# Performance work log

Hardware: AMD Instinct MI355X
Metric: run time of the kernel (lower is better)

## Reference

```python
import jax, jax.numpy as jnp
import numpy as np

OUT_F, IN_F = 4096, 11008
NUMEL = OUT_F * IN_F            # divisible by 256
NUM_SUPER = NUMEL // 256        # super-blocks of 8 sub-blocks x 32 values


def setup_inputs() -> dict:
    key = jax.random.key(0)
    k = jax.random.split(key, 7)
    x = jax.random.normal(k[0], (64, IN_F), dtype=jnp.float32)
    packed = jax.random.randint(k[1], (NUMEL // 2,), 0, 256, dtype=jnp.int32)
    d = jax.random.uniform(k[2], (NUM_SUPER,), dtype=jnp.float32) * 0.02
    dmin = jax.random.uniform(k[3], (NUM_SUPER,), dtype=jnp.float32) * 0.02
    scales = jax.random.randint(k[4], (NUM_SUPER * 8,), 0, 64, dtype=jnp.int32)
    mins = jax.random.randint(k[5], (NUM_SUPER * 8,), 0, 64, dtype=jnp.int32)
    bias = jax.random.normal(k[6], (OUT_F,), dtype=jnp.float32) * 0.02
    return {"x": x, "packed": packed, "d": d, "dmin": dmin,
            "scales": scales, "mins": mins, "bias": bias}


def _dequant_q4k(packed, d, dmin, scales, mins):
    # unpack two 4-bit quants per byte, interleaved low/high (stack dim=1 + flatten)
    low = packed & 15
    high = (packed >> 4) & 15
    q = jnp.stack([low, high], axis=1).reshape(NUM_SUPER, 8, 32).astype(jnp.float32)
    sc = (scales.astype(jnp.float32) / 63.0).reshape(NUM_SUPER, 8, 1)
    mn = (mins.astype(jnp.float32) / 63.0).reshape(NUM_SUPER, 8, 1)
    normalized = q / 15.0 * sc + mn
    w = normalized * d.reshape(NUM_SUPER, 1, 1) + dmin.reshape(NUM_SUPER, 1, 1)
    return w.reshape(OUT_F, IN_F)


def reference(x, packed, d, dmin, scales, mins, bias):
    w = _dequant_q4k(packed, d, dmin, scales, mins)   # [OUT_F, IN_F] fp32
    return x @ w.T + bias                              # F.linear
```

## Files before the change

kernel.cpp:

```cpp
#include <hip/hip_runtime.h>
#include <stdint.h>

#define OUT_F   4096
#define IN_F    11008
#define BATCH   64
#define NSUP    43
#define SB_ROW  344
#define IPR     5504
#define NKS     16
#define XP_BYTES   (4 * 344 * 64 * 16)
#define PART_ELEMS ((size_t)NKS * BATCH * OUT_F)
#define WS_FULL    (XP_BYTES + PART_ELEMS * 4)

typedef __attribute__((ext_vector_type(8))) short  short8;
typedef __attribute__((ext_vector_type(4))) float  floatx4;
typedef __attribute__((ext_vector_type(4))) int    intx4;

__device__ __forceinline__ unsigned pack_bf16(float f0, float f1) {
    return __builtin_amdgcn_perm(__float_as_uint(f1), __float_as_uint(f0), 0x07060302u);
}

__global__ __launch_bounds__(256) void xprep_kernel(const float* __restrict__ x,
                                                    intx4* __restrict__ xp) {
    const int ksb = blockIdx.x;
    const int mt  = threadIdx.x >> 6;
    const int l   = threadIdx.x & 63;
    const int lo  = l & 15, hi = l >> 4;
    const float* src = x + (mt * 16 + lo) * IN_F + ksb * 32 + hi * 8;
    floatx4 a0 = *(const floatx4*)src;
    floatx4 a1 = *(const floatx4*)(src + 4);
    intx4 r;
    r.x = pack_bf16(a0.x, a0.y);
    r.y = pack_bf16(a0.z, a0.w);
    r.z = pack_bf16(a1.x, a1.y);
    r.w = pack_bf16(a1.z, a1.w);
    xp[(mt * 344 + ksb) * 64 + l] = r;
}

__global__ __launch_bounds__(256) void init_out_kernel(const float* __restrict__ bias,
                                                       float* __restrict__ out) {
    int i = blockIdx.x * 256 + threadIdx.x;
    out[i] = bias[i & (OUT_F - 1)];
}

__global__ __launch_bounds__(256) void reduce_kernel(const float* __restrict__ part,
                                                     const float* __restrict__ bias,
                                                     float* __restrict__ out) {
    const int i = blockIdx.x * 256 + threadIdx.x;
    float s = bias[i & (OUT_F - 1)];
    #pragma unroll
    for (int k = 0; k < NKS; ++k) s += part[(size_t)k * (BATCH * OUT_F) + i];
    out[i] = s;
}

template<bool USE_PART>
__global__ __launch_bounds__(256, 4) void qlin_main(
    const intx4* __restrict__ xp,
    const int*   __restrict__ packed,
    const float* __restrict__ dd,
    const float* __restrict__ dmn_g,
    const int*   __restrict__ scales,
    const int*   __restrict__ mins,
    float*       __restrict__ part,
    float*       __restrict__ out)
{
    const int ks = blockIdx.x & 15;
    const int nb = blockIdx.x >> 4;
    const int w  = threadIdx.x >> 6;
    const int l  = threadIdx.x & 63;
    const int lo = l & 15, hi = l >> 4;

    const int o    = nb * 64 + w * 16 + lo;
    const int sup0 = ks < 11 ? 3 * ks : 33 + 2 * (ks - 11);
    const int nsup = ks < 11 ? 3 : 2;

    floatx4 acc[4];
    #pragma unroll
    for (int mt = 0; mt < 4; ++mt) acc[mt] = (floatx4)0.0f;

    const int* bp  = packed + o * IPR + sup0 * 128 + hi * 4;
    const int* scp = scales + o * SB_ROW + sup0 * 8;
    const int* mnp = mins   + o * SB_ROW + sup0 * 8;
    int didx = o * NSUP + sup0;
    const intx4* xpc = xp + (sup0 * 8) * 64 + l;

    intx4 bc[4], bn[4], scc, mnc, scn, mnn;
    #pragma unroll
    for (int i = 0; i < 4; ++i)
        bc[i] = __builtin_nontemporal_load((const intx4*)(bp + i * 16));
    scc = *(const intx4*)scp;
    mnc = *(const intx4*)mnp;
    float dvc = dd[didx], dmc = dmn_g[didx];

    auto do_half = [&](const intx4* bb, intx4 scv, intx4 mnv,
                       float A945, float A63, float ADMN, const intx4* xq) {
        #pragma unroll
        for (int st = 0; st < 4; ++st) {
            const int v0 = bb[st].x, v1 = bb[st].y, v2 = bb[st].z, v3 = bb[st].w;
            const float A = A945 * (float)scv[st];
            const float B = fmaf(A63, (float)mnv[st], ADMN);
            union { intx4 i; short8 s; } uw;
            uw.i.x = pack_bf16(fmaf((float)(v0 & 15), A, B), fmaf((float)(v0 >> 4), A, B));
            uw.i.y = pack_bf16(fmaf((float)(v1 & 15), A, B), fmaf((float)(v1 >> 4), A, B));
            uw.i.z = pack_bf16(fmaf((float)(v2 & 15), A, B), fmaf((float)(v2 >> 4), A, B));
            uw.i.w = pack_bf16(fmaf((float)(v3 & 15), A, B), fmaf((float)(v3 >> 4), A, B));
            union { intx4 i; short8 s; } u0, u1, u2, u3;
            u0.i = xq[(0 * 344 + st) * 64];
            u1.i = xq[(1 * 344 + st) * 64];
            u2.i = xq[(2 * 344 + st) * 64];
            u3.i = xq[(3 * 344 + st) * 64];
            acc[0] = __builtin_amdgcn_mfma_f32_16x16x32_bf16(u0.s, uw.s, acc[0], 0, 0, 0);
            acc[1] = __builtin_amdgcn_mfma_f32_16x16x32_bf16(u1.s, uw.s, acc[1], 0, 0, 0);
            acc[2] = __builtin_amdgcn_mfma_f32_16x16x32_bf16(u2.s, uw.s, acc[2], 0, 0, 0);
            acc[3] = __builtin_amdgcn_mfma_f32_16x16x32_bf16(u3.s, uw.s, acc[3], 0, 0, 0);
        }
    };

    #pragma unroll 1
    for (int s = 0;; ++s) {
        const bool last = (s == nsup - 1);
        #pragma unroll
        for (int i = 0; i < 4; ++i)
            bn[i] = __builtin_nontemporal_load((const intx4*)(bp + 64 + i * 16));
        scn = *(const intx4*)(scp + 4);
        mnn = *(const intx4*)(mnp + 4);

        const float A945 = dvc * (1.0f / 945.0f);
        const float A63  = dvc * (1.0f / 63.0f);
        do_half(bc, scc, mnc, A945, A63, dmc, xpc);

        float dvn = 0.0f, dmnn = 0.0f;
        if (!last) {
            #pragma unroll
            for (int i = 0; i < 4; ++i)
                bc[i] = __builtin_nontemporal_load((const intx4*)(bp + 128 + i * 16));
            scc = *(const intx4*)(scp + 8);
            mnc = *(const intx4*)(mnp + 8);
            dvn = dd[didx + 1];
            dmnn = dmn_g[didx + 1];
        }
        do_half(bn, scn, mnn, A945, A63, dmc, xpc + 256);
        if (last) break;
        dvc = dvn; dmc = dmnn; ++didx;
        bp += 128; scp += 8; mnp += 8; xpc += 512;
    }

    if (USE_PART) {
        float* pbase = part + (size_t)ks * (BATCH * OUT_F) + o;
        #pragma unroll
        for (int mt = 0; mt < 4; ++mt) {
            #pragma unroll
            for (int r = 0; r < 4; ++r)
                pbase[(mt * 16 + hi * 4 + r) * OUT_F] = acc[mt][r];
        }
    } else {
        #pragma unroll
        for (int mt = 0; mt < 4; ++mt) {
            #pragma unroll
            for (int r = 0; r < 4; ++r)
                atomicAdd(out + (mt * 16 + hi * 4 + r) * OUT_F + o, acc[mt][r]);
        }
    }
}

extern "C" void kernel_launch(void* const* d_in, const int* in_sizes, int n_in,
                              void* d_out, int out_size, void* d_ws, size_t ws_size,
                              hipStream_t stream) {
    (void)in_sizes; (void)n_in; (void)out_size;
    const float* x      = (const float*)d_in[0];
    const int*   packed = (const int*)d_in[1];
    const float* d      = (const float*)d_in[2];
    const float* dmin   = (const float*)d_in[3];
    const int*   scales = (const int*)d_in[4];
    const int*   mins   = (const int*)d_in[5];
    const float* bias   = (const float*)d_in[6];
    float* out = (float*)d_out;

    const bool has_part = ws_size >= (size_t)WS_FULL;
    intx4* xp   = (intx4*)d_ws;
    float* part = (float*)((char*)d_ws + XP_BYTES);

    xprep_kernel<<<344, 256, 0, stream>>>(x, xp);

    if (has_part) {
        qlin_main<true><<<64 * NKS, 256, 0, stream>>>(
            xp, packed, d, dmin, scales, mins, part, out);
        reduce_kernel<<<(BATCH * OUT_F) / 256, 256, 0, stream>>>(part, bias, out);
    } else {
        init_out_kernel<<<(BATCH * OUT_F) / 256, 256, 0, stream>>>(bias, out);
        qlin_main<false><<<64 * NKS, 256, 0, stream>>>(
            xp, packed, d, dmin, scales, mins, part, out);
    }
}
```

Before: 181.5 us.

## Batch-load full super-block of weights and activations per iteration, halve occupancy

Replaces the register double-buffered half-superblock pipeline with a loop that issues all 8 weight loads and all 32 activation fragment loads for a super-block up front, then runs dequant and MFMA. This raises memory-level parallelism per wave and front-loads the activation reads that were previously interleaved with MFMAs. Launch bounds drop from 4 to 2 waves per SIMD to make room for the larger register footprint, which lowers occupancy. Loads for the next super-block no longer overlap with compute on the current one.

```diff
diff --git a/kernel.cpp b/kernel.cpp
--- a/kernel.cpp
+++ b/kernel.cpp
@@ -54,7 +54,7 @@
 }
 
 template<bool USE_PART>
-__global__ __launch_bounds__(256, 4) void qlin_main(
+__global__ __launch_bounds__(256, 2) void qlin_main(
     const intx4* __restrict__ xp,
     const int*   __restrict__ packed,
     const float* __restrict__ dd,
@@ -74,75 +74,66 @@
     const int sup0 = ks < 11 ? 3 * ks : 33 + 2 * (ks - 11);
     const int nsup = ks < 11 ? 3 : 2;
 
+    const int*   bp0  = packed + o * IPR + sup0 * 128 + hi * 4;
+    const intx4* xq0  = xp + (sup0 * 8) * 64 + l;
+    const int*   scp0 = scales + o * SB_ROW + sup0 * 8;
+    const int*   mnp0 = mins   + o * SB_ROW + sup0 * 8;
+    const int    didx0 = o * NSUP + sup0;
+
     floatx4 acc[4];
     #pragma unroll
     for (int mt = 0; mt < 4; ++mt) acc[mt] = (floatx4)0.0f;
 
-    const int* bp  = packed + o * IPR + sup0 * 128 + hi * 4;
-    const int* scp = scales + o * SB_ROW + sup0 * 8;
-    const int* mnp = mins   + o * SB_ROW + sup0 * 8;
-    int didx = o * NSUP + sup0;
-    const intx4* xpc = xp + (sup0 * 8) * 64 + l;
+    #pragma unroll 1
+    for (int s = 0; s < nsup; ++s) {
+        const int*   bp = bp0 + s * 128;
+        const intx4* xq = xq0 + s * 512;
 
-    intx4 bc[4], bn[4], scc, mnc, scn, mnn;
-    #pragma unroll
-    for (int i = 0; i < 4; ++i)
-        bc[i] = __builtin_nontemporal_load((const intx4*)(bp + i * 16));
-    scc = *(const intx4*)scp;
-    mnc = *(const intx4*)mnp;
-    float dvc = dd[didx], dmc = dmn_g[didx];
+        intx4 br[8];
+        #pragma unroll
+        for (int st = 0; st < 8; ++st)
+            br[st] = __builtin_nontemporal_load((const intx4*)(bp + st * 16));
 
-    auto do_half = [&](const intx4* bb, intx4 scv, intx4 mnv,
-                       float A945, float A63, float ADMN, const intx4* xq) {
+        intx4 xf[32];
         #pragma unroll
-        for (int st = 0; st < 4; ++st) {
-            const int v0 = bb[st].x, v1 = bb[st].y, v2 = bb[st].z, v3 = bb[st].w;
-            const float A = A945 * (float)scv[st];
-            const float B = fmaf(A63, (float)mnv[st], ADMN);
-            union { intx4 i; short8 s; } uw;
+        for (int mt = 0; mt < 4; ++mt) {
+            #pragma unroll
+            for (int st = 0; st < 8; ++st)
+                xf[mt * 8 + st] = xq[(mt * 344 + st) * 64];
+        }
+
+        const intx4 sc0 = *(const intx4*)(scp0 + s * 8);
+        const intx4 sc1 = *(const intx4*)(scp0 + s * 8 + 4);
+        const intx4 mn0 = *(const intx4*)(mnp0 + s * 8);
+        const intx4 mn1 = *(const intx4*)(mnp0 + s * 8 + 4);
+        const float dv  = dd[didx0 + s];
+        const float dmv = dmn_g[didx0 + s];
+        const float A945 = dv * (1.0f / 945.0f);
+        const float A63  = dv * (1.0f / 63.0f);
+
+        #pragma unroll
+        for (int st = 0; st < 8; ++st) {
+            const int scv = (st < 4) ? sc0[st & 3] : sc1[st & 3];
+            const int mnv = (st < 4) ? mn0[st & 3] : mn1[st & 3];
+            const float A = A945 * (float)scv;
+            const float B = fmaf(A63, (float)mnv, dmv);
+            const int v0 = br[st].x, v1 = br[st].y, v2 = br[st].z, v3 = br[st].w;
+            union { intx4 i; short8 s8; } uw;
             uw.i.x = pack_bf16(fmaf((float)(v0 & 15), A, B), fmaf((float)(v0 >> 4), A, B));
             uw.i.y = pack_bf16(fmaf((float)(v1 & 15), A, B), fmaf((float)(v1 >> 4), A, B));
             uw.i.z = pack_bf16(fmaf((float)(v2 & 15), A, B), fmaf((float)(v2 >> 4), A, B));
             uw.i.w = pack_bf16(fmaf((float)(v3 & 15), A, B), fmaf((float)(v3 >> 4), A, B));
-            union { intx4 i; short8 s; } u0, u1, u2, u3;
-            u0.i = xq[(0 * 344 + st) * 64];
-            u1.i = xq[(1 * 344 + st) * 64];
-            u2.i = xq[(2 * 344 + st) * 64];
-            u3.i = xq[(3 * 344 + st) * 64];
-            acc[0] = __builtin_amdgcn_mfma_f32_16x16x32_bf16(u0.s, uw.s, acc[0], 0, 0, 0);
-            acc[1] = __builtin_amdgcn_mfma_f32_16x16x32_bf16(u1.s, uw.s, acc[1], 0, 0, 0);
-            acc[2] = __builtin_amdgcn_mfma_f32_16x16x32_bf16(u2.s, uw.s, acc[2], 0, 0, 0);
-            acc[3] = __builtin_amdgcn_mfma_f32_16x16x32_bf16(u3.s, uw.s, acc[3], 0, 0, 0);
+
+            union { intx4 i; short8 s8; } u0, u1, u2, u3;
+            u0.i = xf[0 * 8 + st];
+            u1.i = xf[1 * 8 + st];
+            u2.i = xf[2 * 8 + st];
+            u3.i = xf[3 * 8 + st];
+            acc[0] = __builtin_amdgcn_mfma_f32_16x16x32_bf16(u0.s8, uw.s8, acc[0], 0, 0, 0);
+            acc[1] = __builtin_amdgcn_mfma_f32_16x16x32_bf16(u1.s8, uw.s8, acc[1], 0, 0, 0);
+            acc[2] = __builtin_amdgcn_mfma_f32_16x16x32_bf16(u2.s8, uw.s8, acc[2], 0, 0, 0);
+            acc[3] = __builtin_amdgcn_mfma_f32_16x16x32_bf16(u3.s8, uw.s8, acc[3], 0, 0, 0);
         }
-    };
-
-    #pragma unroll 1
-    for (int s = 0;; ++s) {
-        const bool last = (s == nsup - 1);
-        #pragma unroll
-        for (int i = 0; i < 4; ++i)
-            bn[i] = __builtin_nontemporal_load((const intx4*)(bp + 64 + i * 16));
-        scn = *(const intx4*)(scp + 4);
-        mnn = *(const intx4*)(mnp + 4);
-
-        const float A945 = dvc * (1.0f / 945.0f);
-        const float A63  = dvc * (1.0f / 63.0f);
-        do_half(bc, scc, mnc, A945, A63, dmc, xpc);
-
-        float dvn = 0.0f, dmnn = 0.0f;
-        if (!last) {
-            #pragma unroll
-            for (int i = 0; i < 4; ++i)
-                bc[i] = __builtin_nontemporal_load((const intx4*)(bp + 128 + i * 16));
-            scc = *(const intx4*)(scp + 8);
-            mnc = *(const intx4*)(mnp + 8);
-            dvn = dd[didx + 1];
-            dmnn = dmn_g[didx + 1];
-        }
-        do_half(bn, scn, mnn, A945, A63, dmc, xpc + 256);
-        if (last) break;
-        dvc = dvn; dmc = dmnn; ++didx;
-        bp += 128; scp += 8; mnp += 8; xpc += 512;
     }
 
     if (USE_PART) {
```

Result: no change. 181.3 us (-0.1%).
